# Performance work log

Measured on AMD Instinct MI355X. Metric: run time of the kernel, lower is better.

Reference implementation:

```python
import jax, jax.numpy as jnp
import numpy as np

P = 3  # cubic B-spline degree
N_KNOTS = 8
LATENT = 32


def _de_boor(x, t, c):
    # Vectorized de Boor: digitize -> gather control points -> 3-level blend.
    k = jnp.digitize(x, t) - 1
    d = [c[j + k - P] for j in range(P + 1)]
    for r in range(1, P + 1):
        for j in range(P, r - 1, -1):
            alpha = (x - t[j + k - P]) / (t[j + 1 + k - r] - t[j + k - P])
            d[j] = (1.0 - alpha) * d[j - 1] + alpha * d[j]
    return d[P]


def setup_inputs() -> dict:
    key = jax.random.key(0)
    ks = jax.random.split(key, 10)
    f32 = jnp.float32
    x = jax.random.uniform(ks[0], (256, 256, 256), dtype=f32)
    a = jax.random.uniform(ks[1], (1,), dtype=f32)
    # Dense params (lecun-normal-ish init, zero bias like flax defaults)
    W1 = jax.random.normal(ks[2], (1, LATENT), f32)
    b1 = jnp.zeros((LATENT,), f32)
    W2 = jax.random.normal(ks[3], (LATENT, LATENT), f32) / np.sqrt(LATENT)
    b2 = jnp.zeros((LATENT,), f32)
    Ww = jax.random.normal(ks[4], (LATENT, N_KNOTS + 1), f32) / np.sqrt(LATENT)
    bw = jnp.zeros((N_KNOTS + 1,), f32)
    Wk = jax.random.normal(ks[5], (LATENT, N_KNOTS - 1), f32) / np.sqrt(LATENT)
    bk = jnp.zeros((N_KNOTS - 1,), f32)
    return {"x": x, "a": a, "W1": W1, "b1": b1, "W2": W2, "b2": b2,
            "Ww": Ww, "bw": bw, "Wk": Wk, "bk": bk}


def reference(x, a, W1, b1, W2, b2, Ww, bw, Wk, bk):
    a_vec = jnp.atleast_1d(a)
    net = jnp.sin(a_vec @ W1 + b1)
    net = jnp.sin(net @ W2 + b2)
    w = net @ Ww + bw                      # (n_knots+1,)
    kraw = net @ Wk + bk                   # (n_knots-1,)
    kpos = jnp.concatenate([jnp.zeros((1,), x.dtype),
                            jnp.cumsum(jax.nn.softmax(kraw))])
    w = jnp.concatenate([jnp.zeros((1,), x.dtype), w])
    ak = jnp.concatenate([jnp.zeros((3,), x.dtype), kpos, jnp.ones((3,), x.dtype)])
    xp = jnp.clip(x / jnp.sqrt(jnp.asarray(3.0, x.dtype)), 0.0, 1.0 - 0.0001)
    return _de_boor(xp, ak, w)
```

## Files before the change

kernel.cpp:

```cpp
#include <hip/hip_runtime.h>


#define ITERS 8

typedef float floatx4 __attribute__((ext_vector_type(4)));

__global__ __launch_bounds__(256) void nsff_fused_kernel(
    const float4* __restrict__ x, float4* __restrict__ out,
    const float* __restrict__ a,
    const float* __restrict__ W1, const float* __restrict__ b1,
    const float* __restrict__ W2, const float* __restrict__ b2,
    const float* __restrict__ Ww, const float* __restrict__ bw,
    const float* __restrict__ Wk, const float* __restrict__ bk) {
    __shared__ float net1[32];
    __shared__ float net2[32];
    __shared__ float w9s[9];
    __shared__ float kraws[7];
    __shared__ float tsh[14];
    __shared__ float w10s[10];
    __shared__ float4 tbl[7];
    __shared__ float csh[6];

    const int tid = threadIdx.x;
    const int stride = gridDim.x * 256;
    const int base = blockIdx.x * 256 + tid;

    float a0 = 0.f, w1v = 0.f, b1v = 0.f;
    if (tid < 32) { a0 = a[0]; w1v = W1[tid]; b1v = b1[tid]; }

    float4 xv[ITERS];
#pragma unroll
    for (int it = 0; it < ITERS; ++it) xv[it] = x[base + it * stride];
    asm volatile("" ::: "memory");

    if (tid < 32) net1[tid] = sinf(a0 * w1v + b1v);
    if (tid < 32) {
        float s = b2[tid];
#pragma unroll 16
        for (int j = 0; j < 32; ++j) s += net1[j] * W2[j * 32 + tid];
        net2[tid] = sinf(s);
    }
    if (tid < 9) {
        float s = bw[tid];
#pragma unroll
        for (int j = 0; j < 32; ++j) s += net2[j] * Ww[j * 9 + tid];
        w9s[tid] = s;
    } else if (tid >= 16 && tid < 23) {
        const int i = tid - 16;
        float s = bk[i];
#pragma unroll
        for (int j = 0; j < 32; ++j) s += net2[j] * Wk[j * 7 + i];
        kraws[i] = s;
    }
    if (tid == 0) {
        float mx = kraws[0];
        for (int i = 1; i < 7; ++i) mx = fmaxf(mx, kraws[i]);
        float e[7], sum = 0.f;
        for (int i = 0; i < 7; ++i) { e[i] = expf(kraws[i] - mx); sum += e[i]; }
        const float invsum = 1.f / sum;
        tsh[0] = tsh[1] = tsh[2] = tsh[3] = 0.f;
        float cs = 0.f;
        for (int i = 0; i < 7; ++i) { cs += e[i] * invsum; tsh[4 + i] = cs; }
        tsh[11] = tsh[12] = tsh[13] = 1.f;
        w10s[0] = 0.f;
        for (int i = 0; i < 9; ++i) w10s[1 + i] = w9s[i];
        for (int i = 0; i < 6; ++i) csh[i] = tsh[4 + i];
    }
    if (tid < 7) {
        const int k = tid + 3;
        float d[4][4];
        for (int j = 0; j < 4; ++j) {
            d[j][0] = w10s[k - 3 + j];
            d[j][1] = 0.f; d[j][2] = 0.f; d[j][3] = 0.f;
        }
        for (int r = 1; r <= 3; ++r) {
            for (int j = 3; j >= r; --j) {
                const float t0 = tsh[j + k - 3];
                const float t1 = tsh[j + 1 + k - r];
                const float den = t1 - t0;
                const float invd = (den != 0.f) ? (1.f / den) : 0.f;
                const float a0_ = (tsh[k] - t0) * invd;
                float nd[4];
                for (int i = 0; i < 4; ++i) nd[i] = d[j - 1][i] + a0_ * (d[j][i] - d[j - 1][i]);
                for (int i = 0; i < 3; ++i) nd[i + 1] += invd * (d[j][i] - d[j - 1][i]);
                for (int i = 0; i < 4; ++i) d[j][i] = nd[i];
            }
        }
        tbl[tid] = make_float4(d[3][0], d[3][1], d[3][2], d[3][3]);
    }
    __syncthreads();

    float cs[6];
#pragma unroll
    for (int i = 0; i < 6; ++i) cs[i] = csh[i];

#pragma unroll
    for (int it = 0; it < ITERS; ++it) {
        floatx4 r;
#pragma unroll
        for (int c = 0; c < 4; ++c) {
            const float xi = (&xv[it].x)[c];
            const float xp = __builtin_amdgcn_fmed3f(
                xi * 0.57735026918962576f, 0.0f, 0.9999f);
            int kk = 0;
            float tk = 0.f;
#pragma unroll
            for (int i = 0; i < 6; ++i) {
                if (xp >= cs[i]) { kk = i + 1; tk = cs[i]; }
            }
            const float s = xp - tk;
            const float4 cf = tbl[kk];
            r[c] = fmaf(fmaf(fmaf(cf.w, s, cf.z), s, cf.y), s, cf.x);
        }
        __builtin_nontemporal_store(
            r, reinterpret_cast<floatx4*>(&out[base + it * stride]));
    }
}

__global__ __launch_bounds__(256) void nsff_tail_kernel(
    const float4* __restrict__ x, float4* __restrict__ out, int n4, int start,
    const float* __restrict__ ws_dummy) {  }

extern "C" void kernel_launch(void* const* d_in, const int* in_sizes, int n_in,
                              void* d_out, int out_size, void* d_ws, size_t ws_size,
                              hipStream_t stream) {
    const float* x  = (const float*)d_in[0];
    const float* a  = (const float*)d_in[1];
    const float* W1 = (const float*)d_in[2];
    const float* b1 = (const float*)d_in[3];
    const float* W2 = (const float*)d_in[4];
    const float* b2 = (const float*)d_in[5];
    const float* Ww = (const float*)d_in[6];
    const float* bw = (const float*)d_in[7];
    const float* Wk = (const float*)d_in[8];
    const float* bk = (const float*)d_in[9];
    float* out = (float*)d_out;

    const int n4 = out_size / 4;
    const int blocks = n4 / (256 * ITERS);
    nsff_fused_kernel<<<blocks, 256, 0, stream>>>((const float4*)x, (float4*)out,
                                                  a, W1, b1, W2, b2, Ww, bw, Wk, bk);
}
```

Baseline: 132.8 us.

## Split tiny MLP/spline table setup into a single-block precompute kernel

Moves the per-block MLP evaluation, softmax knot computation and polynomial coefficient table construction into a one-block kernel that writes the table to workspace. The streaming kernel then only loads 34 floats per block instead of recomputing the MLP in every block. This removes redundant per-block setup work and its serial latency, at the cost of an extra kernel launch and a dependency between the two launches. The old fused kernel is kept as a fallback when no workspace is available.

```diff
diff --git a/kernel.cpp b/kernel.cpp
--- a/kernel.cpp
+++ b/kernel.cpp
@@ -4,6 +4,127 @@
 #define ITERS 8
 
 typedef float floatx4 __attribute__((ext_vector_type(4)));
+
+__global__ __launch_bounds__(64) void nsff_table_kernel(
+    float* __restrict__ ws,
+    const float* __restrict__ a,
+    const float* __restrict__ W1, const float* __restrict__ b1,
+    const float* __restrict__ W2, const float* __restrict__ b2,
+    const float* __restrict__ Ww, const float* __restrict__ bw,
+    const float* __restrict__ Wk, const float* __restrict__ bk) {
+    __shared__ float net1[32];
+    __shared__ float net2[32];
+    __shared__ float w9s[9];
+    __shared__ float kraws[7];
+    __shared__ float tsh[14];
+    __shared__ float w10s[10];
+
+    const int tid = threadIdx.x;
+    if (tid < 32) net1[tid] = sinf(a[0] * W1[tid] + b1[tid]);
+    if (tid < 32) {
+        float s = b2[tid];
+#pragma unroll 16
+        for (int j = 0; j < 32; ++j) s += net1[j] * W2[j * 32 + tid];
+        net2[tid] = sinf(s);
+    }
+    if (tid < 9) {
+        float s = bw[tid];
+#pragma unroll
+        for (int j = 0; j < 32; ++j) s += net2[j] * Ww[j * 9 + tid];
+        w9s[tid] = s;
+    } else if (tid >= 16 && tid < 23) {
+        const int i = tid - 16;
+        float s = bk[i];
+#pragma unroll
+        for (int j = 0; j < 32; ++j) s += net2[j] * Wk[j * 7 + i];
+        kraws[i] = s;
+    }
+    if (tid == 0) {
+        float mx = kraws[0];
+        for (int i = 1; i < 7; ++i) mx = fmaxf(mx, kraws[i]);
+        float e[7], sum = 0.f;
+        for (int i = 0; i < 7; ++i) { e[i] = expf(kraws[i] - mx); sum += e[i]; }
+        const float invsum = 1.f / sum;
+        tsh[0] = tsh[1] = tsh[2] = tsh[3] = 0.f;
+        float cs = 0.f;
+        for (int i = 0; i < 7; ++i) { cs += e[i] * invsum; tsh[4 + i] = cs; }
+        tsh[11] = tsh[12] = tsh[13] = 1.f;
+        w10s[0] = 0.f;
+        for (int i = 0; i < 9; ++i) w10s[1 + i] = w9s[i];
+        for (int i = 0; i < 6; ++i) ws[28 + i] = tsh[4 + i];
+    }
+    if (tid < 7) {
+        const int k = tid + 3;
+        float d[4][4];
+        for (int j = 0; j < 4; ++j) {
+            d[j][0] = w10s[k - 3 + j];
+            d[j][1] = 0.f; d[j][2] = 0.f; d[j][3] = 0.f;
+        }
+        for (int r = 1; r <= 3; ++r) {
+            for (int j = 3; j >= r; --j) {
+                const float t0 = tsh[j + k - 3];
+                const float t1 = tsh[j + 1 + k - r];
+                const float den = t1 - t0;
+                const float invd = (den != 0.f) ? (1.f / den) : 0.f;
+                const float a0_ = (tsh[k] - t0) * invd;
+                float nd[4];
+                for (int i = 0; i < 4; ++i) nd[i] = d[j - 1][i] + a0_ * (d[j][i] - d[j - 1][i]);
+                for (int i = 0; i < 3; ++i) nd[i + 1] += invd * (d[j][i] - d[j - 1][i]);
+                for (int i = 0; i < 4; ++i) d[j][i] = nd[i];
+            }
+        }
+        ws[4 * tid + 0] = d[3][0];
+        ws[4 * tid + 1] = d[3][1];
+        ws[4 * tid + 2] = d[3][2];
+        ws[4 * tid + 3] = d[3][3];
+    }
+}
+
+__global__ __launch_bounds__(256) void nsff_main_kernel(
+    const float4* __restrict__ x, float4* __restrict__ out,
+    const float* __restrict__ ws) {
+    __shared__ float4 tbl[7];
+    __shared__ float csh[6];
+
+    const int tid = threadIdx.x;
+    if (tid < 7) tbl[tid] = reinterpret_cast<const float4*>(ws)[tid];
+    if (tid >= 16 && tid < 22) csh[tid - 16] = ws[28 + (tid - 16)];
+    __syncthreads();
+
+    const int stride = gridDim.x * 256;
+    const int base = blockIdx.x * 256 + tid;
+
+    float4 xv[ITERS];
+#pragma unroll
+    for (int it = 0; it < ITERS; ++it) xv[it] = x[base + it * stride];
+    asm volatile("" ::: "memory");
+
+    float cs[6];
+#pragma unroll
+    for (int i = 0; i < 6; ++i) cs[i] = csh[i];
+
+#pragma unroll
+    for (int it = 0; it < ITERS; ++it) {
+        floatx4 r;
+#pragma unroll
+        for (int c = 0; c < 4; ++c) {
+            const float xi = (&xv[it].x)[c];
+            const float xp = __builtin_amdgcn_fmed3f(
+                xi * 0.57735026918962576f, 0.0f, 0.9999f);
+            int kk = 0;
+            float tk = 0.f;
+#pragma unroll
+            for (int i = 0; i < 6; ++i) {
+                if (xp >= cs[i]) { kk = i + 1; tk = cs[i]; }
+            }
+            const float s = xp - tk;
+            const float4 cf = tbl[kk];
+            r[c] = fmaf(fmaf(fmaf(cf.w, s, cf.z), s, cf.y), s, cf.x);
+        }
+        __builtin_nontemporal_store(
+            r, reinterpret_cast<floatx4*>(&out[base + it * stride]));
+    }
+}
 
 __global__ __launch_bounds__(256) void nsff_fused_kernel(
     const float4* __restrict__ x, float4* __restrict__ out,
@@ -117,10 +238,6 @@
     }
 }
 
-__global__ __launch_bounds__(256) void nsff_tail_kernel(
-    const float4* __restrict__ x, float4* __restrict__ out, int n4, int start,
-    const float* __restrict__ ws_dummy) {  }
-
 extern "C" void kernel_launch(void* const* d_in, const int* in_sizes, int n_in,
                               void* d_out, int out_size, void* d_ws, size_t ws_size,
                               hipStream_t stream) {
@@ -138,6 +255,16 @@
 
     const int n4 = out_size / 4;
     const int blocks = n4 / (256 * ITERS);
-    nsff_fused_kernel<<<blocks, 256, 0, stream>>>((const float4*)x, (float4*)out,
-                                                  a, W1, b1, W2, b2, Ww, bw, Wk, bk);
-}
+
+    if (d_ws != nullptr && ws_size >= 34 * sizeof(float)) {
+        float* ws = (float*)d_ws;
+        nsff_table_kernel<<<1, 64, 0, stream>>>(ws, a, W1, b1, W2, b2,
+                                                Ww, bw, Wk, bk);
+        nsff_main_kernel<<<blocks, 256, 0, stream>>>((const float4*)x,
+                                                     (float4*)out, ws);
+    } else {
+        nsff_fused_kernel<<<blocks, 256, 0, stream>>>((const float4*)x,
+                                                      (float4*)out, a, W1, b1,
+                                                      W2, b2, Ww, bw, Wk, bk);
+    }
+}
```

Result: no change. 132.1 us (-0.5%).

## Compute spline table per wavefront and drop block barrier, prefetch two chunks ahead

Applied to the files above, without the earlier changes.

Each of the four wavefronts now computes the MLP, knot positions and polynomial table redundantly in its own shared-memory slot, so the block-wide __syncthreads is removed. Without the barrier, each wave can start streaming as soon as its own table is ready instead of waiting on the slowest wave. The eight up-front x loads are replaced by a rolling two-ahead prefetch, which lowers register pressure but keeps fewer loads in flight. Correctness relies on lanes of a single wave seeing each other's shared-memory writes without a barrier, which is implicit and fragile.

```diff
diff --git a/kernel.cpp b/kernel.cpp
--- a/kernel.cpp
+++ b/kernel.cpp
@@ -1,105 +1,111 @@
 #include <hip/hip_runtime.h>
 
 
-#define ITERS 8
+#define CHUNKS 8
 
 typedef float floatx4 __attribute__((ext_vector_type(4)));
 
-__global__ __launch_bounds__(256) void nsff_fused_kernel(
+__global__ __launch_bounds__(256) void nsff_fused_nb_kernel(
     const float4* __restrict__ x, float4* __restrict__ out,
     const float* __restrict__ a,
     const float* __restrict__ W1, const float* __restrict__ b1,
     const float* __restrict__ W2, const float* __restrict__ b2,
     const float* __restrict__ Ww, const float* __restrict__ bw,
     const float* __restrict__ Wk, const float* __restrict__ bk) {
-    __shared__ float net1[32];
-    __shared__ float net2[32];
-    __shared__ float w9s[9];
-    __shared__ float kraws[7];
-    __shared__ float tsh[14];
-    __shared__ float w10s[10];
-    __shared__ float4 tbl[7];
-    __shared__ float csh[6];
+    __shared__ float net1s[4][32];
+    __shared__ float net2s[4][32];
+    __shared__ float w9ss[4][9];
+    __shared__ float krawss[4][7];
+    __shared__ float tshs[4][14];
+    __shared__ float w10ss[4][10];
+    __shared__ float tblws[4][28];
 
     const int tid = threadIdx.x;
+    const int wid = tid >> 6;
+    const int lane = tid & 63;
+
     const int stride = gridDim.x * 256;
     const int base = blockIdx.x * 256 + tid;
 
     float a0 = 0.f, w1v = 0.f, b1v = 0.f;
-    if (tid < 32) { a0 = a[0]; w1v = W1[tid]; b1v = b1[tid]; }
+    if (lane < 32) { a0 = a[0]; w1v = W1[lane]; b1v = b1[lane]; }
 
-    float4 xv[ITERS];
-#pragma unroll
-    for (int it = 0; it < ITERS; ++it) xv[it] = x[base + it * stride];
+    float4 cur = x[base];
+    float4 nxt = x[base + stride];
     asm volatile("" ::: "memory");
 
-    if (tid < 32) net1[tid] = sinf(a0 * w1v + b1v);
-    if (tid < 32) {
-        float s = b2[tid];
+    if (lane < 32) net1s[wid][lane] = sinf(a0 * w1v + b1v);
+    if (lane < 32) {
+        float s = b2[lane];
 #pragma unroll 16
-        for (int j = 0; j < 32; ++j) s += net1[j] * W2[j * 32 + tid];
-        net2[tid] = sinf(s);
+        for (int j = 0; j < 32; ++j) s += net1s[wid][j] * W2[j * 32 + lane];
+        net2s[wid][lane] = sinf(s);
     }
-    if (tid < 9) {
-        float s = bw[tid];
+    if (lane < 9) {
+        float s = bw[lane];
 #pragma unroll
-        for (int j = 0; j < 32; ++j) s += net2[j] * Ww[j * 9 + tid];
-        w9s[tid] = s;
-    } else if (tid >= 16 && tid < 23) {
-        const int i = tid - 16;
+        for (int j = 0; j < 32; ++j) s += net2s[wid][j] * Ww[j * 9 + lane];
+        w9ss[wid][lane] = s;
+    } else if (lane >= 16 && lane < 23) {
+        const int i = lane - 16;
         float s = bk[i];
 #pragma unroll
-        for (int j = 0; j < 32; ++j) s += net2[j] * Wk[j * 7 + i];
-        kraws[i] = s;
+        for (int j = 0; j < 32; ++j) s += net2s[wid][j] * Wk[j * 7 + i];
+        krawss[wid][i] = s;
     }
-    if (tid == 0) {
-        float mx = kraws[0];
-        for (int i = 1; i < 7; ++i) mx = fmaxf(mx, kraws[i]);
+    if (lane == 0) {
+        float mx = krawss[wid][0];
+        for (int i = 1; i < 7; ++i) mx = fmaxf(mx, krawss[wid][i]);
         float e[7], sum = 0.f;
-        for (int i = 0; i < 7; ++i) { e[i] = expf(kraws[i] - mx); sum += e[i]; }
+        for (int i = 0; i < 7; ++i) { e[i] = expf(krawss[wid][i] - mx); sum += e[i]; }
         const float invsum = 1.f / sum;
-        tsh[0] = tsh[1] = tsh[2] = tsh[3] = 0.f;
-        float cs = 0.f;
-        for (int i = 0; i < 7; ++i) { cs += e[i] * invsum; tsh[4 + i] = cs; }
-        tsh[11] = tsh[12] = tsh[13] = 1.f;
-        w10s[0] = 0.f;
-        for (int i = 0; i < 9; ++i) w10s[1 + i] = w9s[i];
-        for (int i = 0; i < 6; ++i) csh[i] = tsh[4 + i];
+        tshs[wid][0] = tshs[wid][1] = tshs[wid][2] = tshs[wid][3] = 0.f;
+        float cum = 0.f;
+        for (int i = 0; i < 7; ++i) { cum += e[i] * invsum; tshs[wid][4 + i] = cum; }
+        tshs[wid][11] = tshs[wid][12] = tshs[wid][13] = 1.f;
+        w10ss[wid][0] = 0.f;
+        for (int i = 0; i < 9; ++i) w10ss[wid][1 + i] = w9ss[wid][i];
     }
-    if (tid < 7) {
-        const int k = tid + 3;
+    if (lane < 7) {
+        const int k = lane + 3;
         float d[4][4];
         for (int j = 0; j < 4; ++j) {
-            d[j][0] = w10s[k - 3 + j];
+            d[j][0] = w10ss[wid][k - 3 + j];
             d[j][1] = 0.f; d[j][2] = 0.f; d[j][3] = 0.f;
         }
         for (int r = 1; r <= 3; ++r) {
             for (int j = 3; j >= r; --j) {
-                const float t0 = tsh[j + k - 3];
-                const float t1 = tsh[j + 1 + k - r];
+                const float t0 = tshs[wid][j + k - 3];
+                const float t1 = tshs[wid][j + 1 + k - r];
                 const float den = t1 - t0;
                 const float invd = (den != 0.f) ? (1.f / den) : 0.f;
-                const float a0_ = (tsh[k] - t0) * invd;
+                const float a0_ = (tshs[wid][k] - t0) * invd;
                 float nd[4];
                 for (int i = 0; i < 4; ++i) nd[i] = d[j - 1][i] + a0_ * (d[j][i] - d[j - 1][i]);
                 for (int i = 0; i < 3; ++i) nd[i + 1] += invd * (d[j][i] - d[j - 1][i]);
                 for (int i = 0; i < 4; ++i) d[j][i] = nd[i];
             }
         }
-        tbl[tid] = make_float4(d[3][0], d[3][1], d[3][2], d[3][3]);
+        tblws[wid][4 * lane + 0] = d[3][0];
+        tblws[wid][4 * lane + 1] = d[3][1];
+        tblws[wid][4 * lane + 2] = d[3][2];
+        tblws[wid][4 * lane + 3] = d[3][3];
     }
-    __syncthreads();
 
+    const float4* tbl = reinterpret_cast<const float4*>(tblws[wid]);
     float cs[6];
 #pragma unroll
-    for (int i = 0; i < 6; ++i) cs[i] = csh[i];
+    for (int i = 0; i < 6; ++i) cs[i] = tshs[wid][4 + i];
 
 #pragma unroll
-    for (int it = 0; it < ITERS; ++it) {
+    for (int it = 0; it < CHUNKS; ++it) {
+        float4 fol;
+        if (it + 2 < CHUNKS) fol = x[base + (it + 2) * stride];
+
         floatx4 r;
 #pragma unroll
         for (int c = 0; c < 4; ++c) {
-            const float xi = (&xv[it].x)[c];
+            const float xi = (&cur.x)[c];
             const float xp = __builtin_amdgcn_fmed3f(
                 xi * 0.57735026918962576f, 0.0f, 0.9999f);
             int kk = 0;
@@ -114,12 +120,11 @@
         }
         __builtin_nontemporal_store(
             r, reinterpret_cast<floatx4*>(&out[base + it * stride]));
+
+        cur = nxt;
+        nxt = fol;
     }
 }
-
-__global__ __launch_bounds__(256) void nsff_tail_kernel(
-    const float4* __restrict__ x, float4* __restrict__ out, int n4, int start,
-    const float* __restrict__ ws_dummy) {  }
 
 extern "C" void kernel_launch(void* const* d_in, const int* in_sizes, int n_in,
                               void* d_out, int out_size, void* d_ws, size_t ws_size,
@@ -137,7 +142,9 @@
     float* out = (float*)d_out;
 
     const int n4 = out_size / 4;
-    const int blocks = n4 / (256 * ITERS);
-    nsff_fused_kernel<<<blocks, 256, 0, stream>>>((const float4*)x, (float4*)out,
-                                                  a, W1, b1, W2, b2, Ww, bw, Wk, bk);
+    const int blocks = n4 / (256 * CHUNKS);
+
+    nsff_fused_nb_kernel<<<blocks, 256, 0, stream>>>((const float4*)x,
+                                                     (float4*)out, a, W1, b1,
+                                                     W2, b2, Ww, bw, Wk, bk);
 }
```

New measurement: 133.0 us. About the same (+0.1%).
